# Performance work log

Hardware: AMD Instinct MI355X
Metric: run time of the kernel (lower is better)

The kernel has to match this reference:

```python
import jax, jax.numpy as jnp
import numpy as np

K = 3
STRIDE = 1
PAD = K // 2
GN_GROUPS = 32
EPS = 1e-5


def _conv(x, w, b, stride, pad):
    y = jax.lax.conv_general_dilated(
        x, w, window_strides=(stride, stride),
        padding=[(pad, pad), (pad, pad)],
        dimension_numbers=("NCHW", "OIHW", "NCHW"))
    return y + b[None, :, None, None]


def _bilinear_gather(img, ys, xs):
    # img: [B,C,H,W]; ys/xs: [B,P,Ho,Wo] float sampling coords (zero padding outside)
    B, C, H, W = img.shape
    y0 = jnp.floor(ys)
    x0 = jnp.floor(xs)
    y1, x1 = y0 + 1.0, x0 + 1.0
    wy1 = ys - y0  # weight toward y1
    wx1 = xs - x0
    wy0 = 1.0 - wy1
    wx0 = 1.0 - wx1
    img_flat = img.reshape(B, C, H * W)

    def corner(yc, xc, wgt):
        yi = yc.astype(jnp.int32)
        xi = xc.astype(jnp.int32)
        valid = (yi >= 0) & (yi < H) & (xi >= 0) & (xi < W)
        idx = jnp.clip(yi, 0, H - 1) * W + jnp.clip(xi, 0, W - 1)  # [B,P,Ho,Wo]
        Bp, P, Ho, Wo = idx.shape
        idx_f = jnp.broadcast_to(idx.reshape(B, 1, P * Ho * Wo), (B, C, P * Ho * Wo))
        vals = jnp.take_along_axis(img_flat, idx_f, axis=2).reshape(B, C, P, Ho, Wo)
        w_eff = jnp.where(valid, wgt, 0.0)[:, None]  # [B,1,P,Ho,Wo]
        return vals * w_eff

    out = (corner(y0, x0, wy0 * wx0) + corner(y0, x1, wy0 * wx1)
           + corner(y1, x0, wy1 * wx0) + corner(y1, x1, wy1 * wx1))
    return out  # [B,C,P,Ho,Wo]


def _deform_conv_gn_relu(x, w_off, b_off, w, b, gamma, beta):
    B, C_in, H, W = x.shape
    C_out = w.shape[0]
    P = K * K
    # offset-predicting conv: [B, 2*P, Ho, Wo], channel order (dy0,dx0,dy1,dx1,...)
    off = _conv(x, w_off, b_off, STRIDE, PAD)
    Ho, Wo = off.shape[2], off.shape[3]
    off = off.reshape(B, P, 2, Ho, Wo)
    dy, dx = off[:, :, 0], off[:, :, 1]  # [B,P,Ho,Wo]
    ky, kx = jnp.meshgrid(jnp.arange(K, dtype=x.dtype), jnp.arange(K, dtype=x.dtype), indexing="ij")
    ky, kx = ky.reshape(P), kx.reshape(P)
    base_y = (jnp.arange(Ho, dtype=x.dtype) * STRIDE - PAD)
    base_x = (jnp.arange(Wo, dtype=x.dtype) * STRIDE - PAD)
    ys = base_y[None, None, :, None] + ky[None, :, None, None] + dy
    xs = base_x[None, None, None, :] + kx[None, :, None, None] + dx
    cols = _bilinear_gather(x, ys, xs)  # [B,C_in,P,Ho,Wo]
    y = jnp.einsum("bcphw,ocp->bohw", cols, w.reshape(C_out, C_in, P)) + b[None, :, None, None]
    # GroupNorm(32, C_out)
    G = GN_GROUPS
    yg = y.reshape(B, G, (C_out // G) * Ho * Wo)
    mu = yg.mean(axis=2, keepdims=True)
    var = yg.var(axis=2, keepdims=True)
    yn = ((yg - mu) * jax.lax.rsqrt(var + EPS)).reshape(B, C_out, Ho, Wo)
    yn = yn * gamma[None, :, None, None] + beta[None, :, None, None]
    return jax.nn.relu(yn)


def setup_inputs() -> dict:
    key = jax.random.key(0)
    ks = jax.random.split(key, 7)
    B, C_in, C_out, H, W = 4, 256, 256, 64, 64
    P = K * K
    fan = C_in * P
    x = jax.random.normal(ks[0], (B, C_in, H, W), dtype=jnp.float32)
    w_off = jax.random.normal(ks[1], (2 * P, C_in, K, K), dtype=jnp.float32) * 0.01
    b_off = jnp.zeros((2 * P,), dtype=jnp.float32)
    w = jax.random.normal(ks[2], (C_out, C_in, K, K), dtype=jnp.float32) / np.sqrt(fan)
    b = jax.random.normal(ks[3], (C_out,), dtype=jnp.float32) * 0.01
    gamma = jnp.ones((C_out,), dtype=jnp.float32)
    beta = jnp.zeros((C_out,), dtype=jnp.float32)
    return {"x": x, "w_off": w_off, "b_off": b_off, "w": w, "b": b, "gamma": gamma, "beta": beta}


def reference(x, w_off, b_off, w, b, gamma, beta):
    return _deform_conv_gn_relu(x, w_off, b_off, w, b, gamma, beta)
```

## Files before the change

### kernel.cpp

```cpp
#include <hip/hip_runtime.h>
#include <hip/hip_bf16.h>

using bf16 = __hip_bfloat16;
typedef __attribute__((ext_vector_type(4))) float f32x4;
typedef __attribute__((ext_vector_type(2))) float f32x2;
typedef __attribute__((ext_vector_type(8))) __bf16 bf16x8;
typedef __attribute__((ext_vector_type(4))) __bf16 bf16x4;

#define CIN 256
#define COUT 256
#define HW 4096
#define NB 4
#define NTOT 16384
#define KDIM 2304

__global__ __launch_bounds__(256) void k_pre(const float* __restrict__ x,
                                             const float* __restrict__ w,
                                             const float* __restrict__ wof,
                                             bf16* __restrict__ xt,
                                             bf16* __restrict__ A,
                                             float* __restrict__ wt) {
  int bid = blockIdx.x;
  int tid = threadIdx.x;
  if (bid < 2048) {
    __shared__ float t[64][33];
    int ct = bid & 3;
    int hwt = (bid >> 2) & 127;
    int b = bid >> 9;
    int c0 = ct * 64, hw0 = hwt * 32;
    const float* xb = x + (size_t)b * CIN * HW;
    int cc = tid >> 5, ww = tid & 31;
#pragma unroll
    for (int pass = 0; pass < 8; ++pass)
      t[cc + pass * 8][ww] = xb[(size_t)(c0 + cc + pass * 8) * HW + hw0 + ww];
    __syncthreads();
    int hwl = tid >> 3, ce = (tid & 7) * 8;
    bf16x8 v;
#pragma unroll
    for (int e = 0; e < 8; ++e) v[e] = (__bf16)t[ce + e][hwl];
    *(bf16x8*)(xt + ((size_t)b * HW + hw0 + hwl) * CIN + c0 + ce) = v;
  } else if (bid < 4352) {
    int i = (bid - 2048) * 256 + tid;
    int o = i / KDIM, r = i % KDIM;
    int p = r >> 8, c = r & 255;
    A[i] = __float2bfloat16(w[((size_t)o * 256 + c) * 9 + p]);
  } else {
    int i = (bid - 4352) * 256 + tid;
    if (i < 18 * CIN * 9) {
      int oc = i % 18;
      int cp = i / 18;
      int c = cp / 9, p = cp % 9;
      wt[i] = wof[((size_t)oc * CIN + c) * 9 + p];
    }
  }
}

__global__ __launch_bounds__(256) void k_convoff2(const float* __restrict__ x,
                                                  const float* __restrict__ wt,
                                                  float* __restrict__ part) {
  __shared__ float lds[8][6][68];
  int bid = blockIdx.x;
  int chunk = bid & 7;
  int rt = (bid >> 3) & 15;
  int b = bid >> 7;
  int tid = threadIdx.x;
  int wq = tid & 63, r = tid >> 6;
  int h0 = rt * 4;
  int c0 = chunk * 32;

  if (tid < 96) {
    int cl = tid / 12, rem = tid % 12;
    lds[cl][rem >> 1][(rem & 1) ? 66 : 1] = 0.f;
  }

  float acc[18];
#pragma unroll
  for (int o = 0; o < 18; ++o) acc[o] = 0.f;

  int ch = tid >> 5, l32 = tid & 31;
  const float* xb = x + (size_t)b * CIN * HW;

  for (int cs = 0; cs < 32; cs += 8) {
    __syncthreads();
    const float* xp = xb + (size_t)(c0 + cs + ch) * HW;
#pragma unroll
    for (int r6 = 0; r6 < 6; ++r6) {
      int hh = h0 - 1 + r6;
      f32x2 v = {0.f, 0.f};
      if ((unsigned)hh < 64u) v = *(const f32x2*)(xp + hh * 64 + l32 * 2);
      *(f32x2*)&lds[ch][r6][2 + l32 * 2] = v;
    }
    __syncthreads();
#pragma unroll
    for (int cl = 0; cl < 8; ++cl) {
      int c = c0 + cs + cl;
      const float* wc = wt + (size_t)c * 9 * 18;
      float xv[9];
#pragma unroll
      for (int ky = 0; ky < 3; ++ky)
#pragma unroll
        for (int kx = 0; kx < 3; ++kx)
          xv[ky * 3 + kx] = lds[cl][r + ky][1 + wq + kx];
#pragma unroll
      for (int p = 0; p < 9; ++p)
#pragma unroll
        for (int o = 0; o < 18; ++o)
          acc[o] = fmaf(xv[p], wc[p * 18 + o], acc[o]);
    }
  }

  float* pp = part + (size_t)chunk * (NB * 18 * HW) + (size_t)b * 18 * HW +
              (h0 + r) * 64 + wq;
#pragma unroll
  for (int o = 0; o < 18; ++o) pp[(size_t)o * HW] = acc[o];
}

__global__ __launch_bounds__(256) void k_offreduce(const float* __restrict__ part,
                                                   const float* __restrict__ boff,
                                                   float* __restrict__ off) {
  int i = blockIdx.x * 256 + threadIdx.x;
  int e0 = i * 4;
  int oc = (e0 >> 12) % 18;
  float bo = boff[oc];
  f32x4 s = {bo, bo, bo, bo};
#pragma unroll
  for (int c = 0; c < 8; ++c) s += *(const f32x4*)(part + (size_t)c * (NB * 18 * HW) + e0);
  *(f32x4*)(off + e0) = s;
}

__global__ __launch_bounds__(256) void k_gather(const bf16* __restrict__ xt,
                                                const float* __restrict__ off,
                                                bf16* __restrict__ colsT) {
  int tid = threadIdx.x;
  int wv = tid >> 6, l = tid & 63;
  int n = blockIdx.x * 4 + wv;
  int hw = n & 4095;
  int b = n >> 12;
  int h = hw >> 6, wq = hw & 63;
  const bf16* xtb = xt + (size_t)b * HW * CIN + l * 4;
  const float* offb = off + (size_t)b * 18 * HW + hw;
  bf16* outp = colsT + (size_t)n * KDIM + l * 4;
#pragma unroll
  for (int p = 0; p < 9; ++p) {
    float dy = offb[(size_t)(2 * p) * HW];
    float dx = offb[(size_t)(2 * p + 1) * HW];
    float ysf = (float)(h - 1 + p / 3) + dy;
    float xsf = (float)(wq - 1 + p % 3) + dx;
    float y0f = floorf(ysf), x0f = floorf(xsf);
    float wy1 = ysf - y0f, wx1 = xsf - x0f;
    float wy0 = 1.f - wy1, wx0 = 1.f - wx1;
    int y0 = (int)y0f, x0 = (int)x0f;
    int y1 = y0 + 1, x1 = x0 + 1;
    float w00 = wy0 * wx0, w01 = wy0 * wx1, w10 = wy1 * wx0, w11 = wy1 * wx1;
    bool vy0 = (unsigned)y0 < 64u, vy1 = (unsigned)y1 < 64u;
    bool vx0 = (unsigned)x0 < 64u, vx1 = (unsigned)x1 < 64u;
    w00 = (vy0 && vx0) ? w00 : 0.f;
    w01 = (vy0 && vx1) ? w01 : 0.f;
    w10 = (vy1 && vx0) ? w10 : 0.f;
    w11 = (vy1 && vx1) ? w11 : 0.f;
    int y0c = min(max(y0, 0), 63), y1c = min(max(y1, 0), 63);
    int x0c = min(max(x0, 0), 63), x1c = min(max(x1, 0), 63);
    bf16x4 c00 = *(const bf16x4*)(xtb + (size_t)(y0c * 64 + x0c) * CIN);
    bf16x4 c01 = *(const bf16x4*)(xtb + (size_t)(y0c * 64 + x1c) * CIN);
    bf16x4 c10 = *(const bf16x4*)(xtb + (size_t)(y1c * 64 + x0c) * CIN);
    bf16x4 c11 = *(const bf16x4*)(xtb + (size_t)(y1c * 64 + x1c) * CIN);
    bf16x4 o;
#pragma unroll
    for (int k = 0; k < 4; ++k) {
      float v = w00 * (float)c00[k] + w01 * (float)c01[k] +
                w10 * (float)c10[k] + w11 * (float)c11[k];
      o[k] = (__bf16)v;
    }
    *(bf16x4*)(outp + p * 256) = o;
  }
}

__global__ __launch_bounds__(256) void k_gemm(const bf16* __restrict__ A,
                                              const bf16* __restrict__ Bt,
                                              const float* __restrict__ bias,
                                              bf16* __restrict__ Y0,
                                              bf16* __restrict__ Y1) {
  __shared__ bf16 As[2][256 * 64];
  __shared__ bf16 Bs[2][64 * 64];
  int bid = blockIdx.x;
  int swz = (bid & 7) * 64 + (bid >> 3);
  int n0 = (swz >> 1) * 64;
  int khalf = swz & 1;
  int tid = threadIdx.x;
  int lane = tid & 63;
  int wave = tid >> 6;
  int wr = wave * 64;
  f32x4 acc[4][4];
#pragma unroll
  for (int i = 0; i < 4; ++i)
#pragma unroll
    for (int j = 0; j < 4; ++j) acc[i][j] = (f32x4){0.f, 0.f, 0.f, 0.f};

  int srow = tid >> 3;
  int skdst = (tid & 7) * 8;
  int sksrc = ((tid & 7) ^ ((tid >> 3) & 7)) * 8;
  int kbase = khalf * 18;
  auto stage = [&](int buf, int kt) {
    int k0 = (kbase + kt) * 64;
#pragma unroll
    for (int ps = 0; ps < 8; ++ps) {
      int r = srow + ps * 32;
      __builtin_amdgcn_global_load_lds(
          (const __attribute__((address_space(1))) void*)(A + (size_t)r * KDIM + k0 + sksrc),
          (__attribute__((address_space(3))) void*)(&As[buf][r * 64 + skdst]), 16, 0, 0);
    }
#pragma unroll
    for (int ps = 0; ps < 2; ++ps) {
      int r = srow + ps * 32;
      __builtin_amdgcn_global_load_lds(
          (const __attribute__((address_space(1))) void*)(Bt + (size_t)(n0 + r) * KDIM + k0 + sksrc),
          (__attribute__((address_space(3))) void*)(&Bs[buf][r * 64 + skdst]), 16, 0, 0);
    }
  };

  stage(0, 0);
  int rl = lane & 15;
  int kb = (lane >> 4) * 8;
  int xorv = (rl & 7) * 8;
  for (int kt = 0; kt < 18; ++kt) {
    __syncthreads();
    if (kt + 1 < 18) stage((kt + 1) & 1, kt + 1);
    const bf16* as = As[kt & 1];
    const bf16* bs = Bs[kt & 1];
#pragma unroll
    for (int kh = 0; kh < 2; ++kh) {
      int kc = (kh * 32 + kb) ^ xorv;
      bf16x8 af[4], bfr[4];
#pragma unroll
      for (int i = 0; i < 4; ++i)
        af[i] = *(const bf16x8*)(as + (wr + i * 16 + rl) * 64 + kc);
#pragma unroll
      for (int j = 0; j < 4; ++j)
        bfr[j] = *(const bf16x8*)(bs + (j * 16 + rl) * 64 + kc);
#pragma unroll
      for (int i = 0; i < 4; ++i)
#pragma unroll
        for (int j = 0; j < 4; ++j)
          acc[i][j] = __builtin_amdgcn_mfma_f32_16x16x32_bf16(af[i], bfr[j], acc[i][j], 0, 0, 0);
    }
  }

  int cl = lane & 15, rg = (lane >> 4) * 4;
  bf16* Yp = khalf ? Y1 : Y0;
#pragma unroll
  for (int i = 0; i < 4; ++i) {
    int ob = wr + i * 16 + rg;
#pragma unroll
    for (int j = 0; j < 4; ++j) {
      int nn = n0 + j * 16 + cl;
#pragma unroll
      for (int r = 0; r < 4; ++r) {
        float yv = acc[i][j][r] + (khalf ? 0.f : bias[ob + r]);
        Yp[(size_t)(ob + r) * NTOT + nn] = __float2bfloat16(yv);
      }
    }
  }
}

__global__ __launch_bounds__(256) void k_gnstats(const bf16* __restrict__ Y0,
                                                 const bf16* __restrict__ Y1,
                                                 float* __restrict__ mu_,
                                                 float* __restrict__ rs_) {
  int b = blockIdx.x >> 5, g = blockIdx.x & 31;
  int tid = threadIdx.x;
  float s = 0.f, s2 = 0.f;
  for (int i = tid; i < 4096; i += 256) {
    int ol = i >> 9, pos = i & 511;
    size_t off = (size_t)(g * 8 + ol) * NTOT + b * HW + pos * 8;
    bf16x8 v0 = *(const bf16x8*)(Y0 + off);
    bf16x8 v1 = *(const bf16x8*)(Y1 + off);
#pragma unroll
    for (int k = 0; k < 8; ++k) {
      float y = (float)v0[k] + (float)v1[k];
      s += y;
      s2 = fmaf(y, y, s2);
    }
  }
#pragma unroll
  for (int o = 32; o > 0; o >>= 1) {
    s += __shfl_down(s, o);
    s2 += __shfl_down(s2, o);
  }
  __shared__ float red[8];
  int wv = tid >> 6;
  if ((tid & 63) == 0) { red[wv] = s; red[wv + 4] = s2; }
  __syncthreads();
  if (tid == 0) {
    float S = red[0] + red[1] + red[2] + red[3];
    float S2 = red[4] + red[5] + red[6] + red[7];
    float mu = S * (1.f / 32768.f);
    float var = S2 * (1.f / 32768.f) - mu * mu;
    mu_[b * 32 + g] = mu;
    rs_[b * 32 + g] = rsqrtf(var + 1e-5f);
  }
}

__global__ __launch_bounds__(256) void k_apply(const bf16* __restrict__ Y0,
                                               const bf16* __restrict__ Y1,
                                               const float* __restrict__ mu_,
                                               const float* __restrict__ rs_,
                                               const float* __restrict__ gamma,
                                               const float* __restrict__ beta,
                                               float* __restrict__ out) {
  int i = blockIdx.x * 256 + threadIdx.x;
  int hw8 = i & 511;
  int o = (i >> 9) & 255;
  int b = i >> 17;
  int g = o >> 3;
  float mu = mu_[b * 32 + g];
  float rs = rs_[b * 32 + g];
  float s = rs * gamma[o];
  float t = beta[o] - mu * s;
  size_t off = (size_t)o * NTOT + b * HW + hw8 * 8;
  bf16x8 v0 = *(const bf16x8*)(Y0 + off);
  bf16x8 v1 = *(const bf16x8*)(Y1 + off);
  float* op = out + ((size_t)b * COUT + o) * HW + hw8 * 8;
  f32x4 r0, r1;
#pragma unroll
  for (int k = 0; k < 4; ++k)
    r0[k] = fmaxf(((float)v0[k] + (float)v1[k]) * s + t, 0.f);
#pragma unroll
  for (int k = 0; k < 4; ++k)
    r1[k] = fmaxf(((float)v0[k + 4] + (float)v1[k + 4]) * s + t, 0.f);
  *(f32x4*)op = r0;
  *(f32x4*)(op + 4) = r1;
}

extern "C" void kernel_launch(void* const* d_in, const int* in_sizes, int n_in,
                              void* d_out, int out_size, void* d_ws, size_t ws_size,
                              hipStream_t stream) {
  const float* x = (const float*)d_in[0];
  const float* w_off = (const float*)d_in[1];
  const float* b_off = (const float*)d_in[2];
  const float* w = (const float*)d_in[3];
  const float* bias = (const float*)d_in[4];
  const float* gamma = (const float*)d_in[5];
  const float* beta = (const float*)d_in[6];
  float* out = (float*)d_out;
  char* ws = (char*)d_ws;

  bf16* xt = (bf16*)(ws);
  float* offb = (float*)(ws + 8388608);
  bf16* Abf = (bf16*)(ws + 8388608 + 1179648);
  bf16* colsT = (bf16*)(ws + 8388608 + 2 * 1179648);
  bf16* Y0 = (bf16*)(ws + 8388608 + 2 * 1179648 + 75497472);
  bf16* Y1 = Y0 + (size_t)COUT * NTOT;
  float* mus = (float*)(ws + 2 * 8388608 + 2 * 1179648 + 75497472 + 8388608);
  float* rss = mus + 128;

  float* wt = (float*)colsT;
  float* part = (float*)((char*)colsT + 262144);

  k_pre<<<4514, 256, 0, stream>>>(x, w, w_off, xt, Abf, wt);
  k_convoff2<<<512, 256, 0, stream>>>(x, wt, part);
  k_offreduce<<<288, 256, 0, stream>>>(part, b_off, offb);
  k_gather<<<4096, 256, 0, stream>>>(xt, offb, colsT);
  k_gemm<<<512, 256, 0, stream>>>(Abf, colsT, bias, Y0, Y1);
  k_gnstats<<<128, 256, 0, stream>>>(Y0, Y1, mus, rss);
  k_apply<<<2048, 256, 0, stream>>>(Y0, Y1, mus, rss, gamma, beta, out);
}
```

Measured before the change: 132.2 us.

## Fuse GroupNorm stats and apply into one cooperative kernel with grid sync

Replaces the separate GN statistics and apply kernels with one cooperative kernel. Each block loads one channel-batch row of Y into registers, atomically accumulates group sums, waits at a grid-wide sync, then normalizes from registers and writes the output. The goal is to read Y once instead of twice and drop a launch. In exchange it adds atomic contention, a grid barrier across 1024 blocks, and a zeroing block added to the pre kernel.

Result: slower. 319.4 us (+141.7%).

```diff
diff --git a/kernel.cpp b/kernel.cpp
--- a/kernel.cpp
+++ b/kernel.cpp
@@ -1,5 +1,8 @@
 #include <hip/hip_runtime.h>
 #include <hip/hip_bf16.h>
+#include <hip/hip_cooperative_groups.h>
+
+namespace cg = cooperative_groups;
 
 using bf16 = __hip_bfloat16;
 typedef __attribute__((ext_vector_type(4))) float f32x4;
@@ -19,7 +22,8 @@
                                              const float* __restrict__ wof,
                                              bf16* __restrict__ xt,
                                              bf16* __restrict__ A,
-                                             float* __restrict__ wt) {
+                                             float* __restrict__ wt,
+                                             float* __restrict__ gstats) {
   int bid = blockIdx.x;
   int tid = threadIdx.x;
   if (bid < 2048) {
@@ -44,7 +48,7 @@
     int o = i / KDIM, r = i % KDIM;
     int p = r >> 8, c = r & 255;
     A[i] = __float2bfloat16(w[((size_t)o * 256 + c) * 9 + p]);
-  } else {
+  } else if (bid < 4514) {
     int i = (bid - 4352) * 256 + tid;
     if (i < 18 * CIN * 9) {
       int oc = i % 18;
@@ -52,6 +56,8 @@
       int c = cp / 9, p = cp % 9;
       wt[i] = wof[((size_t)oc * CIN + c) * 9 + p];
     }
+  } else {
+    gstats[tid] = 0.f;
   }
 }
 
@@ -262,73 +268,62 @@
   }
 }
 
-__global__ __launch_bounds__(256) void k_gnstats(const bf16* __restrict__ Y0,
+__global__ __launch_bounds__(256) void k_gnapply(const bf16* __restrict__ Y0,
                                                  const bf16* __restrict__ Y1,
-                                                 float* __restrict__ mu_,
-                                                 float* __restrict__ rs_) {
-  int b = blockIdx.x >> 5, g = blockIdx.x & 31;
-  int tid = threadIdx.x;
+                                                 const float* __restrict__ gamma,
+                                                 const float* __restrict__ beta,
+                                                 float* gsum, float* gsq,
+                                                 float* __restrict__ out) {
+  int bid = blockIdx.x;
+  int tid = threadIdx.x;
+  int o = bid & 255, b = bid >> 8;
+  int g = o >> 3;
+  size_t off = (size_t)o * NTOT + b * HW + tid * 16;
+  bf16x8 a0 = *(const bf16x8*)(Y0 + off);
+  bf16x8 a1 = *(const bf16x8*)(Y1 + off);
+  bf16x8 b0 = *(const bf16x8*)(Y0 + off + 8);
+  bf16x8 b1 = *(const bf16x8*)(Y1 + off + 8);
+  float y[16];
+#pragma unroll
+  for (int k = 0; k < 8; ++k) y[k] = (float)a0[k] + (float)a1[k];
+#pragma unroll
+  for (int k = 0; k < 8; ++k) y[k + 8] = (float)b0[k] + (float)b1[k];
   float s = 0.f, s2 = 0.f;
-  for (int i = tid; i < 4096; i += 256) {
-    int ol = i >> 9, pos = i & 511;
-    size_t off = (size_t)(g * 8 + ol) * NTOT + b * HW + pos * 8;
-    bf16x8 v0 = *(const bf16x8*)(Y0 + off);
-    bf16x8 v1 = *(const bf16x8*)(Y1 + off);
-#pragma unroll
-    for (int k = 0; k < 8; ++k) {
-      float y = (float)v0[k] + (float)v1[k];
-      s += y;
-      s2 = fmaf(y, y, s2);
-    }
-  }
-#pragma unroll
-  for (int o = 32; o > 0; o >>= 1) {
-    s += __shfl_down(s, o);
-    s2 += __shfl_down(s2, o);
+#pragma unroll
+  for (int k = 0; k < 16; ++k) {
+    s += y[k];
+    s2 = fmaf(y[k], y[k], s2);
+  }
+  int lane = tid & 63, wv = tid >> 6;
+#pragma unroll
+  for (int mk = 1; mk <= 32; mk <<= 1) {
+    s += __shfl_xor(s, mk);
+    s2 += __shfl_xor(s2, mk);
   }
   __shared__ float red[8];
-  int wv = tid >> 6;
-  if ((tid & 63) == 0) { red[wv] = s; red[wv + 4] = s2; }
+  if (lane == 0) { red[wv] = s; red[wv + 4] = s2; }
   __syncthreads();
   if (tid == 0) {
-    float S = red[0] + red[1] + red[2] + red[3];
-    float S2 = red[4] + red[5] + red[6] + red[7];
-    float mu = S * (1.f / 32768.f);
-    float var = S2 * (1.f / 32768.f) - mu * mu;
-    mu_[b * 32 + g] = mu;
-    rs_[b * 32 + g] = rsqrtf(var + 1e-5f);
-  }
-}
-
-__global__ __launch_bounds__(256) void k_apply(const bf16* __restrict__ Y0,
-                                               const bf16* __restrict__ Y1,
-                                               const float* __restrict__ mu_,
-                                               const float* __restrict__ rs_,
-                                               const float* __restrict__ gamma,
-                                               const float* __restrict__ beta,
-                                               float* __restrict__ out) {
-  int i = blockIdx.x * 256 + threadIdx.x;
-  int hw8 = i & 511;
-  int o = (i >> 9) & 255;
-  int b = i >> 17;
-  int g = o >> 3;
-  float mu = mu_[b * 32 + g];
-  float rs = rs_[b * 32 + g];
-  float s = rs * gamma[o];
-  float t = beta[o] - mu * s;
-  size_t off = (size_t)o * NTOT + b * HW + hw8 * 8;
-  bf16x8 v0 = *(const bf16x8*)(Y0 + off);
-  bf16x8 v1 = *(const bf16x8*)(Y1 + off);
-  float* op = out + ((size_t)b * COUT + o) * HW + hw8 * 8;
-  f32x4 r0, r1;
-#pragma unroll
-  for (int k = 0; k < 4; ++k)
-    r0[k] = fmaxf(((float)v0[k] + (float)v1[k]) * s + t, 0.f);
-#pragma unroll
-  for (int k = 0; k < 4; ++k)
-    r1[k] = fmaxf(((float)v0[k + 4] + (float)v1[k + 4]) * s + t, 0.f);
-  *(f32x4*)op = r0;
-  *(f32x4*)(op + 4) = r1;
+    atomicAdd(&gsum[b * 32 + g], red[0] + red[1] + red[2] + red[3]);
+    atomicAdd(&gsq[b * 32 + g], red[4] + red[5] + red[6] + red[7]);
+  }
+  __threadfence();
+  cg::this_grid().sync();
+  volatile float* vs = gsum;
+  volatile float* vq = gsq;
+  float mu = vs[b * 32 + g] * (1.f / 32768.f);
+  float var = vq[b * 32 + g] * (1.f / 32768.f) - mu * mu;
+  float rs = rsqrtf(var + 1e-5f);
+  float sc = rs * gamma[o];
+  float sh = beta[o] - mu * sc;
+  float* op = out + ((size_t)b * COUT + o) * HW + tid * 16;
+#pragma unroll
+  for (int q = 0; q < 4; ++q) {
+    f32x4 r;
+#pragma unroll
+    for (int k = 0; k < 4; ++k) r[k] = fmaxf(y[q * 4 + k] * sc + sh, 0.f);
+    *(f32x4*)(op + q * 4) = r;
+  }
 }
 
 extern "C" void kernel_launch(void* const* d_in, const int* in_sizes, int n_in,
@@ -350,17 +345,22 @@
   bf16* colsT = (bf16*)(ws + 8388608 + 2 * 1179648);
   bf16* Y0 = (bf16*)(ws + 8388608 + 2 * 1179648 + 75497472);
   bf16* Y1 = Y0 + (size_t)COUT * NTOT;
-  float* mus = (float*)(ws + 2 * 8388608 + 2 * 1179648 + 75497472 + 8388608);
-  float* rss = mus + 128;
+  float* gsum = (float*)(ws + 3 * 8388608 + 2 * 1179648 + 75497472);
+  float* gsq = gsum + 128;
 
   float* wt = (float*)colsT;
   float* part = (float*)((char*)colsT + 262144);
 
-  k_pre<<<4514, 256, 0, stream>>>(x, w, w_off, xt, Abf, wt);
+  k_pre<<<4515, 256, 0, stream>>>(x, w, w_off, xt, Abf, wt, gsum);
   k_convoff2<<<512, 256, 0, stream>>>(x, wt, part);
   k_offreduce<<<288, 256, 0, stream>>>(part, b_off, offb);
   k_gather<<<4096, 256, 0, stream>>>(xt, offb, colsT);
   k_gemm<<<512, 256, 0, stream>>>(Abf, colsT, bias, Y0, Y1);
-  k_gnstats<<<128, 256, 0, stream>>>(Y0, Y1, mus, rss);
-  k_apply<<<2048, 256, 0, stream>>>(Y0, Y1, mus, rss, gamma, beta, out);
-}
+
+  const bf16* cY0 = Y0;
+  const bf16* cY1 = Y1;
+  void* args[] = {(void*)&cY0, (void*)&cY1, (void*)&gamma, (void*)&beta,
+                  (void*)&gsum, (void*)&gsq, (void*)&out};
+  hipLaunchCooperativeKernel((const void*)k_gnapply, dim3(1024), dim3(256),
+                             args, 0, stream);
+}
```
